# Kernel optimization log

Hardware: AMD Instinct MI355X
Metric: run time of the kernel (lower is better)

The kernel has to match this reference:

```python
import jax, jax.numpy as jnp
import numpy as np

N_LEVELS = 16
LOG2_T = 19
T = 1 << LOG2_T
BASE = 16
MAXRES = 4096
F = 2
MAXC = 16  # (max_SH_degree+1)^2
PER_LEVEL_SCALE = float(np.exp((np.log(MAXRES) - np.log(BASE)) / (N_LEVELS - 1)))
RES = jnp.asarray([BASE * PER_LEVEL_SCALE ** l for l in range(N_LEVELS)], dtype=jnp.float32)
PRIMES = jnp.array([1, 2654435761, 805459861], dtype=jnp.uint32)
OFFS = jnp.asarray([[(i >> 2) & 1, (i >> 1) & 1, i & 1] for i in range(8)], dtype=jnp.int32)  # (8,3)

C0 = 0.28209479177387814
C1 = 0.4886025119029199
C2 = (1.0925484305920792, -1.0925484305920792, 0.31539156525252005, -1.0925484305920792, 0.5462742152960396)
C3 = (-0.5900435899266435, 2.890611442640554, -0.4570457994644658, 0.3731763325901154, -0.4570457994644658, 1.445305721320277, -0.5900435899266435)


def hash_encode(x, table):
    # x: (N,3) in [0,1]; table: (L,T,F). Multiresolution hash grid (tcnn HashGrid).
    def level(tab, res):
        p = x * res
        p0 = jnp.floor(p)
        w = p - p0                                  # (N,3) trilerp weights
        c = p0.astype(jnp.uint32)[:, None, :] + OFFS[None].astype(jnp.uint32)  # (N,8,3)
        h = (c[..., 0] * PRIMES[0]) ^ (c[..., 1] * PRIMES[1]) ^ (c[..., 2] * PRIMES[2])
        idx = (h & jnp.uint32(T - 1)).astype(jnp.int32)
        f = tab[idx]                                # (N,8,F) irregular gather
        wc = jnp.where(OFFS[None].astype(bool), w[:, None, :], 1.0 - w[:, None, :]).prod(-1)
        return (f * wc[..., None]).sum(1)           # (N,F)
    feats = jax.vmap(level)(table, RES)             # (L,N,F)
    return feats.transpose(1, 0, 2).reshape(x.shape[0], N_LEVELS * F)


def sh_basis(d):
    # real SH basis up to degree 3; d: (N,3) unit vectors -> (N,16)
    x, y, z = d[..., 0], d[..., 1], d[..., 2]
    xx, yy, zz = x * x, y * y, z * z
    xy, yz, xz = x * y, y * z, x * z
    return jnp.stack([
        jnp.full_like(x, C0), -C1 * y, C1 * z, -C1 * x,
        C2[0] * xy, C2[1] * yz, C2[2] * (2 * zz - xx - yy), C2[3] * xz, C2[4] * (xx - yy),
        C3[0] * y * (3 * xx - yy), C3[1] * xy * z, C3[2] * y * (4 * zz - xx - yy),
        C3[3] * z * (2 * zz - 3 * xx - 3 * yy), C3[4] * x * (4 * zz - xx - yy),
        C3[5] * z * (xx - yy), C3[6] * x * (xx - 3 * yy)], axis=-1)


def network_forward(positions, rx_pos, table, W1, W2, aabb, active_deg):
    aabb_min, aabb_max = aabb[:3], aabb[3:]
    scale = jnp.maximum(aabb_max - aabb_min, 1e-6)
    norm_pos = (positions - aabb_min) / scale
    selector = jnp.all((norm_pos >= 0.0) & (norm_pos <= 1.0), axis=-1)  # (N,)
    pos_n = jnp.clip(norm_pos, 0.0, 1.0)  # safe values for masked-out points (zeroed below)

    def density_fn(pn):
        feats = hash_encode(pn, table)
        h = jax.nn.relu(feats @ W1)
        sh = (h @ W2).reshape(-1, MAXC, 2)
        dens = C0 * sh[:, 0, :]                     # (N,2) = (real, imag) of sigma
        return jnp.sqrt(dens[:, 0] ** 2 + dens[:, 1] ** 2).sum(), (dens, sh)

    # in-forward autograd: grad of sum |sigma| w.r.t. normalized positions
    (_, (dens, sh)), g = jax.value_and_grad(density_fn, has_aux=True)(pos_n)
    g_world = g / scale
    nrm = -g_world / jnp.maximum(jnp.linalg.norm(g_world, axis=-1, keepdims=True), 1e-20)
    nrm = jnp.where(jnp.isnan(nrm), 0.0, nrm)

    # EvalSH: view direction from sample point toward receiver, SH dot coefficients
    dirs = rx_pos - positions
    dirs = dirs / jnp.maximum(jnp.linalg.norm(dirs, axis=-1, keepdims=True), 1e-20)
    Y = sh_basis(dirs)                              # (N,16)
    mask = (jnp.arange(MAXC) < (active_deg + 1) ** 2).astype(Y.dtype)
    scat = jnp.einsum('nc,ncf->nf', Y * mask, sh)   # (N,2) complex as (re,im)

    sel = selector[:, None]
    dens = jnp.where(sel, dens, 0.0)
    scat = jnp.where(sel, scat, 0.0)
    nrm = jnp.where(sel, nrm, 0.0)
    shz = jnp.where(selector[:, None, None], sh, 0.0)
    # pack: sigma(re,im) | scatterers_to(re,im) | normals(3) | sh_coeffs(32) -> (N,39)
    return jnp.concatenate([dens, scat, nrm, shz.reshape(-1, MAXC * 2)], axis=-1)


def setup_inputs() -> dict:
    key = jax.random.key(0)
    ks = jax.random.split(key, 6)
    N = 262144
    positions = jax.random.uniform(ks[0], (N, 3), jnp.float32) * 2.2 - 1.1
    rx_pos = jax.random.normal(ks[1], (3,), jnp.float32) * 2.0
    table = (jax.random.uniform(ks[2], (N_LEVELS, T, F), jnp.float32) * 2.0 - 1.0) * 1e-4
    d_in, hid, d_out = N_LEVELS * F, 32, MAXC * 2
    W1 = jax.random.normal(ks[3], (d_in, hid), jnp.float32) / np.sqrt(d_in)
    W2 = jax.random.normal(ks[4], (hid, d_out), jnp.float32) / np.sqrt(hid)
    aabb = jnp.array([-1.0, -1.0, -1.0, 1.0, 1.0, 1.0], jnp.float32)
    return {"positions": positions, "rx_pos": rx_pos, "table": table, "W1": W1,
            "W2": W2, "aabb": aabb, "active_deg": 3}


def reference(positions, rx_pos, table, W1, W2, aabb, active_deg):
    return network_forward(positions, rx_pos, table, W1, W2, aabb, active_deg)
```

## Files before the change

kernel.cpp:

```cpp
#include <hip/hip_runtime.h>
#include <cmath>

#pragma clang fp contract(off)

#define NLV 16
#define TSZ (1u << 19)
#define TMASK (TSZ - 1u)
#define PR1 2654435761u
#define PR2 805459861u

typedef float v2f __attribute__((ext_vector_type(2)));
typedef float v4f __attribute__((ext_vector_type(4)));

struct ResT { float r[NLV]; };

__device__ __forceinline__ void aabb_norm(
    const float* __restrict__ g_aabb, float posx, float posy, float posz,
    float& s0, float& s1, float& s2,
    float& pnx, float& pny, float& pnz, bool& sel)
{
    float a0 = g_aabb[0], a1 = g_aabb[1], a2 = g_aabb[2];
    s0 = fmaxf(g_aabb[3] - a0, 1e-6f);
    s1 = fmaxf(g_aabb[4] - a1, 1e-6f);
    s2 = fmaxf(g_aabb[5] - a2, 1e-6f);
    float nx = (posx - a0) / s0;
    float ny = (posy - a1) / s1;
    float nz = (posz - a2) / s2;
    sel = (nx >= 0.f) && (nx <= 1.f) && (ny >= 0.f) && (ny <= 1.f)
       && (nz >= 0.f) && (nz <= 1.f);
    pnx = fminf(fmaxf(nx, 0.f), 1.f);
    pny = fminf(fmaxf(ny, 0.f), 1.f);
    pnz = fminf(fmaxf(nz, 0.f), 1.f);
}

__global__ __launch_bounds__(256) void level_gather(
    const float* __restrict__ g_pos,
    const float* __restrict__ g_tab,
    const float* __restrict__ g_aabb,
    float* __restrict__ ws,
    int N, int chunks, ResT rt)
{
    int b = blockIdx.x;
    int lvl = b / chunks;
    int n = (b - lvl * chunks) * 256 + threadIdx.x;
    if (n >= N) return;

    float posx = g_pos[3*n+0], posy = g_pos[3*n+1], posz = g_pos[3*n+2];
    float s0, s1, s2, pnx, pny, pnz; bool sel;
    aabb_norm(g_aabb, posx, posy, posz, s0, s1, s2, pnx, pny, pnz, sel);

    float res = rt.r[lvl];
    const float2* tl = (const float2*)g_tab + (size_t)lvl * TSZ;

    float fx = pnx * res, fy = pny * res, fz = pnz * res;
    float x0 = floorf(fx), y0 = floorf(fy), z0 = floorf(fz);
    float wx = fx - x0, wy = fy - y0, wz = fz - z0;
    float omx = 1.f - wx, omy = 1.f - wy, omz = 1.f - wz;
    unsigned ux = (unsigned)x0, uy = (unsigned)y0, uz = (unsigned)z0;
    unsigned hx0 = ux,        hx1 = ux + 1u;
    unsigned hy0 = uy * PR1,  hy1 = (uy + 1u) * PR1;
    unsigned hz0 = uz * PR2,  hz1 = (uz + 1u) * PR2;
    float f0 = 0.f, f1 = 0.f;
    float lxa = 0.f, lxb = 0.f, lya = 0.f, lyb = 0.f, lza = 0.f, lzb = 0.f;
#pragma unroll
    for (int c = 0; c < 8; ++c) {
        unsigned hh = ((c & 4) ? hx1 : hx0) ^ ((c & 2) ? hy1 : hy0) ^ ((c & 1) ? hz1 : hz0);
        float2 fv = tl[hh & TMASK];
        float wxv = (c & 4) ? wx : omx;
        float wyv = (c & 2) ? wy : omy;
        float wzv = (c & 1) ? wz : omz;
        float wgt = wxv * wyv;
        wgt = wgt * wzv;
        float t0 = fv.x * wgt;
        float t1 = fv.y * wgt;
        f0 = f0 + t0;
        f1 = f1 + t1;
        float pyz = wyv * wzv;
        float pxz = wxv * wzv;
        float pxy = wxv * wyv;
        float spx = (c & 4) ? pyz : -pyz;
        float spy = (c & 2) ? pxz : -pxz;
        float spz = (c & 1) ? pxy : -pxy;
        lxa = lxa + fv.x * spx;  lxb = lxb + fv.y * spx;
        lya = lya + fv.x * spy;  lyb = lyb + fv.y * spy;
        lza = lza + fv.x * spz;  lzb = lzb + fv.y * spz;
    }

    size_t LN = (size_t)NLV * N;
    size_t idx = (size_t)lvl * N + n;
    v2f* f2 = (v2f*)ws;
    v4f* p4 = (v4f*)(ws + 2*LN);
    v2f* p2 = (v2f*)(ws + 6*LN);
    v2f ff = {f0, f1};
    v4f pa = {lxa, lxb, lya, lyb};
    v2f pz = {lza, lzb};
    f2[idx] = ff;
    p4[idx] = pa;
    p2[idx] = pz;
}

__global__ __launch_bounds__(256) void mlp_bwd(
    const float* __restrict__ g_pos,
    const float* __restrict__ g_rx,
    const float* __restrict__ g_W1,
    const float* __restrict__ g_W2,
    const float* __restrict__ g_aabb,
    const int*   __restrict__ g_deg,
    const float* __restrict__ ws,
    float* __restrict__ g_out,
    int N, ResT rt)
{
    int n = blockIdx.x * 256 + threadIdx.x;
    if (n >= N) return;

    float posx = g_pos[3*n+0], posy = g_pos[3*n+1], posz = g_pos[3*n+2];
    float s0, s1, s2, pnx, pny, pnz; bool sel;
    aabb_norm(g_aabb, posx, posy, posz, s0, s1, s2, pnx, pny, pnz, sel);
    (void)pnx; (void)pny; (void)pnz;

    size_t LN = (size_t)NLV * N;
    const v2f* f2 = (const v2f*)ws;
    const v4f* p4 = (const v4f*)(ws + 2*LN);
    const v2f* p2 = (const v2f*)(ws + 6*LN);

    float z1[32];
#pragma unroll
    for (int i = 0; i < 32; ++i) z1[i] = 0.f;
    for (int l = 0; l < NLV; ++l) {
        v2f fv = f2[(size_t)l * N + n];
        float f0 = fv.x;
        float f1 = fv.y;
        const float* w1a = g_W1 + (2*l) * 32;
        const float* w1b = g_W1 + (2*l+1) * 32;
#pragma unroll
        for (int i = 0; i < 32; ++i) {
            float acc = fmaf(f0, w1a[i], z1[i]);
            z1[i] = fmaf(f1, w1b[i], acc);
        }
    }

    unsigned mask = 0u;
    float sh[32];
#pragma unroll
    for (int o = 0; o < 32; ++o) sh[o] = 0.f;
#pragma unroll
    for (int i = 0; i < 32; ++i) {
        bool on = (z1[i] > 0.f);
        if (on) mask |= (1u << i);
        float h = on ? z1[i] : 0.f;
        const float* w2r = g_W2 + i * 32;
#pragma unroll
        for (int o = 0; o < 32; ++o) sh[o] = fmaf(h, w2r[o], sh[o]);
    }

    const float C0c = 0.28209479177387814f;
    float d0 = C0c * sh[0], d1 = C0c * sh[1];

    float rx0 = g_rx[0], rx1 = g_rx[1], rx2 = g_rx[2];
    float dxw = rx0 - posx, dyw = rx1 - posy, dzw = rx2 - posz;
    float dnorm = sqrtf(dxw*dxw + dyw*dyw + dzw*dzw);
    float dinv = 1.f / fmaxf(dnorm, 1e-20f);
    float X = dxw * dinv, Yd = dyw * dinv, Z = dzw * dinv;
    float xx = X*X, yy = Yd*Yd, zz = Z*Z;
    float xy = X*Yd, yz = Yd*Z, xz = X*Z;
    float Yb[16];
    Yb[0]  = 0.28209479177387814f;
    Yb[1]  = -0.4886025119029199f * Yd;
    Yb[2]  =  0.4886025119029199f * Z;
    Yb[3]  = -0.4886025119029199f * X;
    Yb[4]  =  1.0925484305920792f * xy;
    Yb[5]  = -1.0925484305920792f * yz;
    Yb[6]  =  0.31539156525252005f * (2.f*zz - xx - yy);
    Yb[7]  = -1.0925484305920792f * xz;
    Yb[8]  =  0.5462742152960396f * (xx - yy);
    Yb[9]  = -0.5900435899266435f * Yd * (3.f*xx - yy);
    Yb[10] =  2.890611442640554f  * xy * Z;
    Yb[11] = -0.4570457994644658f * Yd * (4.f*zz - xx - yy);
    Yb[12] =  0.3731763325901154f * Z * (2.f*zz - 3.f*xx - 3.f*yy);
    Yb[13] = -0.4570457994644658f * X * (4.f*zz - xx - yy);
    Yb[14] =  1.445305721320277f  * Z * (xx - yy);
    Yb[15] = -0.5900435899266435f * X * (xx - 3.f*yy);

    int deg = g_deg[0];
    int nact = (deg + 1) * (deg + 1);
    float sc0 = 0.f, sc1 = 0.f;
#pragma unroll
    for (int c = 0; c < 16; ++c) {
        float yc = (c < nact) ? Yb[c] : 0.f;
        sc0 = fmaf(yc, sh[2*c+0], sc0);
        sc1 = fmaf(yc, sh[2*c+1], sc1);
    }

    float* op = g_out + (size_t)n * 39;
    op[0] = sel ? d0  : 0.f;
    op[1] = sel ? d1  : 0.f;
    op[2] = sel ? sc0 : 0.f;
    op[3] = sel ? sc1 : 0.f;
#pragma unroll
    for (int c = 0; c < 32; ++c) op[7 + c] = sel ? sh[c] : 0.f;

    float ss = d0*d0 + d1*d1;
    float q0 = 0.f, q1 = 0.f;
    if (ss > 0.f) {
        float sr = sqrtf(ss);
        q0 = C0c * d0 / sr;
        q1 = C0c * d1 / sr;
    }
    float dzv[32];
#pragma unroll
    for (int i = 0; i < 32; ++i) {
        float dh = fmaf(q0, g_W2[i*32+0], q1 * g_W2[i*32+1]);
        dzv[i] = ((mask >> i) & 1u) ? dh : 0.f;
    }

    float gx = 0.f, gy = 0.f, gz = 0.f;
    const float4* w1v = (const float4*)g_W1;
    for (int l = 0; l < NLV; ++l) {
        v4f c4 = p4[(size_t)l * N + n];
        v2f c2 = p2[(size_t)l * N + n];
        const float4* wa = w1v + (size_t)(2*l) * 8;
        const float4* wb = wa + 8;
        float da = 0.f, db = 0.f;
#pragma unroll
        for (int k = 0; k < 8; ++k) {
            float4 va = wa[k], vb = wb[k];
            da = fmaf(va.x, dzv[4*k+0], da);
            da = fmaf(va.y, dzv[4*k+1], da);
            da = fmaf(va.z, dzv[4*k+2], da);
            da = fmaf(va.w, dzv[4*k+3], da);
            db = fmaf(vb.x, dzv[4*k+0], db);
            db = fmaf(vb.y, dzv[4*k+1], db);
            db = fmaf(vb.z, dzv[4*k+2], db);
            db = fmaf(vb.w, dzv[4*k+3], db);
        }
        float res = rt.r[l];
        gx = fmaf(res, fmaf(da, c4.x, db * c4.y), gx);
        gy = fmaf(res, fmaf(da, c4.z, db * c4.w), gy);
        gz = fmaf(res, fmaf(da, c2.x, db * c2.y), gz);
    }

    float gwx = gx / s0, gwy = gy / s1, gwz = gz / s2;
    float gn = sqrtf(gwx*gwx + gwy*gwy + gwz*gwz);
    float ginv = -1.f / fmaxf(gn, 1e-20f);
    op[4] = sel ? gwx * ginv : 0.f;
    op[5] = sel ? gwy * ginv : 0.f;
    op[6] = sel ? gwz * ginv : 0.f;
}

__global__ __launch_bounds__(256, 2) void ngp_fused(
    const float* __restrict__ g_pos,
    const float* __restrict__ g_rx,
    const float* __restrict__ g_tab,
    const float* __restrict__ g_W1,
    const float* __restrict__ g_W2,
    const float* __restrict__ g_aabb,
    const int*   __restrict__ g_deg,
    float* __restrict__ g_out,
    int N, ResT rt)
{
    __shared__ float sm[48][256];

    int tid = blockIdx.x * 256 + threadIdx.x;
    int lt  = threadIdx.x;
    int n = tid >> 1;
    int p = tid & 1;
    if (n >= N) return;

    float posx = g_pos[3*n+0], posy = g_pos[3*n+1], posz = g_pos[3*n+2];
    float s0, s1, s2, pnx, pny, pnz; bool sel;
    aabb_norm(g_aabb, posx, posy, posz, s0, s1, s2, pnx, pny, pnz, sel);

    const float2* tab = (const float2*)g_tab;
    float f0o[8], f1o[8];
#pragma unroll
    for (int j = 0; j < 8; ++j) {
        float res = p ? rt.r[8+j] : rt.r[j];
        const float2* tl = tab + (size_t)(p * 8 + j) * TSZ;
        float fx = pnx * res, fy = pny * res, fz = pnz * res;
        float x0 = floorf(fx), y0 = floorf(fy), z0 = floorf(fz);
        float wx = fx - x0, wy = fy - y0, wz = fz - z0;
        float omx = 1.f - wx, omy = 1.f - wy, omz = 1.f - wz;
        unsigned ux = (unsigned)x0, uy = (unsigned)y0, uz = (unsigned)z0;
        unsigned hx0 = ux,        hx1 = ux + 1u;
        unsigned hy0 = uy * PR1,  hy1 = (uy + 1u) * PR1;
        unsigned hz0 = uz * PR2,  hz1 = (uz + 1u) * PR2;
        float f0 = 0.f, f1 = 0.f;
        float lxa = 0.f, lxb = 0.f, lya = 0.f, lyb = 0.f, lza = 0.f, lzb = 0.f;
#pragma unroll
        for (int c = 0; c < 8; ++c) {
            unsigned hh = ((c & 4) ? hx1 : hx0) ^ ((c & 2) ? hy1 : hy0) ^ ((c & 1) ? hz1 : hz0);
            float2 fv = tl[hh & TMASK];
            float wxv = (c & 4) ? wx : omx;
            float wyv = (c & 2) ? wy : omy;
            float wzv = (c & 1) ? wz : omz;
            float wgt = wxv * wyv;
            wgt = wgt * wzv;
            float t0 = fv.x * wgt;
            float t1 = fv.y * wgt;
            f0 = f0 + t0;
            f1 = f1 + t1;
            float pyz = wyv * wzv;
            float pxz = wxv * wzv;
            float pxy = wxv * wyv;
            float spx = (c & 4) ? pyz : -pyz;
            float spy = (c & 2) ? pxz : -pxz;
            float spz = (c & 1) ? pxy : -pxy;
            lxa = lxa + fv.x * spx;  lxb = lxb + fv.y * spx;
            lya = lya + fv.x * spy;  lyb = lyb + fv.y * spy;
            lza = lza + fv.x * spz;  lzb = lzb + fv.y * spz;
        }
        f0o[j] = f0; f1o[j] = f1;
        sm[j*6+0][lt] = lxa;  sm[j*6+1][lt] = lxb;
        sm[j*6+2][lt] = lya;  sm[j*6+3][lt] = lyb;
        sm[j*6+4][lt] = lza;  sm[j*6+5][lt] = lzb;
    }

    float z1[32];
#pragma unroll
    for (int i = 0; i < 32; ++i) z1[i] = 0.f;
    float hi0[8], hi1[8];
#pragma unroll
    for (int j = 0; j < 8; ++j) {
        float t0 = __shfl_xor(f0o[j], 1, 64);
        float t1 = __shfl_xor(f1o[j], 1, 64);
        float lo0 = p ? t0 : f0o[j];
        float lo1 = p ? t1 : f1o[j];
        hi0[j] = p ? f0o[j] : t0;
        hi1[j] = p ? f1o[j] : t1;
        const float* w1a = g_W1 + (2*j) * 32;
        const float* w1b = g_W1 + (2*j+1) * 32;
#pragma unroll
        for (int i = 0; i < 32; ++i) {
            float acc = fmaf(lo0, w1a[i], z1[i]);
            z1[i] = fmaf(lo1, w1b[i], acc);
        }
    }
#pragma unroll
    for (int j = 0; j < 8; ++j) {
        const float* w1a = g_W1 + (2*(8+j)) * 32;
        const float* w1b = g_W1 + (2*(8+j)+1) * 32;
#pragma unroll
        for (int i = 0; i < 32; ++i) {
            float acc = fmaf(hi0[j], w1a[i], z1[i]);
            z1[i] = fmaf(hi1[j], w1b[i], acc);
        }
    }

    unsigned mask = 0u;
    float sh[32];
#pragma unroll
    for (int o = 0; o < 32; ++o) sh[o] = 0.f;
#pragma unroll
    for (int i = 0; i < 32; ++i) {
        bool on = (z1[i] > 0.f);
        if (on) mask |= (1u << i);
        float h = on ? z1[i] : 0.f;
        const float* w2r = g_W2 + i * 32;
#pragma unroll
        for (int o = 0; o < 32; ++o) sh[o] = fmaf(h, w2r[o], sh[o]);
    }

    const float C0c = 0.28209479177387814f;
    float d0 = C0c * sh[0], d1 = C0c * sh[1];

    float rx0 = g_rx[0], rx1 = g_rx[1], rx2 = g_rx[2];
    float dxw = rx0 - posx, dyw = rx1 - posy, dzw = rx2 - posz;
    float dnorm = sqrtf(dxw*dxw + dyw*dyw + dzw*dzw);
    float dinv = 1.f / fmaxf(dnorm, 1e-20f);
    float X = dxw * dinv, Yd = dyw * dinv, Z = dzw * dinv;
    float xx = X*X, yy = Yd*Yd, zz = Z*Z;
    float xy = X*Yd, yz = Yd*Z, xz = X*Z;
    float Yb[16];
    Yb[0]  = 0.28209479177387814f;
    Yb[1]  = -0.4886025119029199f * Yd;
    Yb[2]  =  0.4886025119029199f * Z;
    Yb[3]  = -0.4886025119029199f * X;
    Yb[4]  =  1.0925484305920792f * xy;
    Yb[5]  = -1.0925484305920792f * yz;
    Yb[6]  =  0.31539156525252005f * (2.f*zz - xx - yy);
    Yb[7]  = -1.0925484305920792f * xz;
    Yb[8]  =  0.5462742152960396f * (xx - yy);
    Yb[9]  = -0.5900435899266435f * Yd * (3.f*xx - yy);
    Yb[10] =  2.890611442640554f  * xy * Z;
    Yb[11] = -0.4570457994644658f * Yd * (4.f*zz - xx - yy);
    Yb[12] =  0.3731763325901154f * Z * (2.f*zz - 3.f*xx - 3.f*yy);
    Yb[13] = -0.4570457994644658f * X * (4.f*zz - xx - yy);
    Yb[14] =  1.445305721320277f  * Z * (xx - yy);
    Yb[15] = -0.5900435899266435f * X * (xx - 3.f*yy);

    int deg = g_deg[0];
    int nact = (deg + 1) * (deg + 1);
    float sc0 = 0.f, sc1 = 0.f;
#pragma unroll
    for (int c = 0; c < 16; ++c) {
        float yc = (c < nact) ? Yb[c] : 0.f;
        sc0 = fmaf(yc, sh[2*c+0], sc0);
        sc1 = fmaf(yc, sh[2*c+1], sc1);
    }

    float* op = g_out + (size_t)n * 39;
    if (p == 0) {
        op[0] = sel ? d0  : 0.f;
        op[1] = sel ? d1  : 0.f;
        op[2] = sel ? sc0 : 0.f;
        op[3] = sel ? sc1 : 0.f;
#pragma unroll
        for (int c = 0; c < 13; ++c) op[7 + c] = sel ? sh[c] : 0.f;
    } else {
#pragma unroll
        for (int c = 13; c < 32; ++c) op[7 + c] = sel ? sh[c] : 0.f;
    }

    float ss = d0*d0 + d1*d1;
    float q0 = 0.f, q1 = 0.f;
    if (ss > 0.f) {
        float sr = sqrtf(ss);
        q0 = C0c * d0 / sr;
        q1 = C0c * d1 / sr;
    }
    float dzv[32];
#pragma unroll
    for (int i = 0; i < 32; ++i) {
        float dh = fmaf(q0, g_W2[i*32+0], q1 * g_W2[i*32+1]);
        dzv[i] = ((mask >> i) & 1u) ? dh : 0.f;
    }

    float gx = 0.f, gy = 0.f, gz = 0.f;
    const float4* w1v = (const float4*)g_W1;
    int rbase = p * 16;
#pragma unroll
    for (int j = 0; j < 8; ++j) {
        const float4* wa = w1v + (size_t)(rbase + 2*j) * 8;
        const float4* wb = wa + 8;
        float da = 0.f, db = 0.f;
#pragma unroll
        for (int k = 0; k < 8; ++k) {
            float4 va = wa[k], vb = wb[k];
            da = fmaf(va.x, dzv[4*k+0], da);
            da = fmaf(va.y, dzv[4*k+1], da);
            da = fmaf(va.z, dzv[4*k+2], da);
            da = fmaf(va.w, dzv[4*k+3], da);
            db = fmaf(vb.x, dzv[4*k+0], db);
            db = fmaf(vb.y, dzv[4*k+1], db);
            db = fmaf(vb.z, dzv[4*k+2], db);
            db = fmaf(vb.w, dzv[4*k+3], db);
        }
        float xa = sm[j*6+0][lt], xb = sm[j*6+1][lt];
        float ya = sm[j*6+2][lt], yb = sm[j*6+3][lt];
        float za = sm[j*6+4][lt], zb = sm[j*6+5][lt];
        float res = p ? rt.r[8+j] : rt.r[j];
        gx = fmaf(res, fmaf(da, xa, db * xb), gx);
        gy = fmaf(res, fmaf(da, ya, db * yb), gy);
        gz = fmaf(res, fmaf(da, za, db * zb), gz);
    }
    float tx = __shfl_xor(gx, 1, 64);
    float ty = __shfl_xor(gy, 1, 64);
    float tz = __shfl_xor(gz, 1, 64);
    gx = gx + tx; gy = gy + ty; gz = gz + tz;

    float gwx = gx / s0, gwy = gy / s1, gwz = gz / s2;
    float gn = sqrtf(gwx*gwx + gwy*gwy + gwz*gwz);
    float ginv = -1.f / fmaxf(gn, 1e-20f);
    if (p == 0) {
        op[4] = sel ? gwx * ginv : 0.f;
        op[5] = sel ? gwy * ginv : 0.f;
        op[6] = sel ? gwz * ginv : 0.f;
    }
}

extern "C" void kernel_launch(void* const* d_in, const int* in_sizes, int n_in,
                              void* d_out, int out_size, void* d_ws, size_t ws_size,
                              hipStream_t stream)
{
    const float* g_pos  = (const float*)d_in[0];
    const float* g_rx   = (const float*)d_in[1];
    const float* g_tab  = (const float*)d_in[2];
    const float* g_W1   = (const float*)d_in[3];
    const float* g_W2   = (const float*)d_in[4];
    const float* g_aabb = (const float*)d_in[5];
    const int*   g_deg  = (const int*)d_in[6];
    float* g_out = (float*)d_out;

    int N = in_sizes[0] / 3;

    ResT rt;
    double scale = exp((log(4096.0) - log(16.0)) / 15.0);
    for (int l = 0; l < NLV; ++l) rt.r[l] = (float)(16.0 * pow(scale, (double)l));

    size_t need = (size_t)NLV * N * 8 * sizeof(float);
    if (ws_size >= need) {
        float* ws = (float*)d_ws;
        int chunks = (N + 255) / 256;
        level_gather<<<NLV * chunks, 256, 0, stream>>>(g_pos, g_tab, g_aabb,
                                                       ws, N, chunks, rt);
        mlp_bwd<<<chunks, 256, 0, stream>>>(g_pos, g_rx, g_W1, g_W2, g_aabb,
                                            g_deg, ws, g_out, N, rt);
    } else {
        long long threads = 2LL * N;
        int blocks = (int)((threads + 255) / 256);
        ngp_fused<<<blocks, 256, 0, stream>>>(g_pos, g_rx, g_tab, g_W1, g_W2,
                                              g_aabb, g_deg, g_out, N, rt);
    }
}
```

Measured before the change: 381.8 us.

## Interleave level blocks, stream workspace stores, and prefetch workspace loads in MLP

The gather kernel now maps consecutive blocks to 8 different levels over the same point chunk, so position loads are shared in cache and eight table slices are gathered concurrently. Workspace writes use nontemporal stores to avoid polluting cache. The MLP/backward kernel issues workspace loads for the first four levels up front and keeps a four-deep rolling prefetch while fully unrolling the level loops, to hide global load latency. The added prefetch registers raise register pressure and may cut occupancy.

```diff
diff --git a/kernel.cpp b/kernel.cpp
--- a/kernel.cpp
+++ b/kernel.cpp
@@ -41,8 +41,10 @@
     int N, int chunks, ResT rt)
 {
     int b = blockIdx.x;
-    int lvl = b / chunks;
-    int n = (b - lvl * chunks) * 256 + threadIdx.x;
+    int half = (b >= 8 * chunks) ? 1 : 0;
+    int bb = b - half * (8 * chunks);
+    int lvl = (bb & 7) + (half << 3);
+    int n = (bb >> 3) * 256 + threadIdx.x;
     if (n >= N) return;
 
     float posx = g_pos[3*n+0], posy = g_pos[3*n+1], posz = g_pos[3*n+2];
@@ -94,9 +96,9 @@
     v2f ff = {f0, f1};
     v4f pa = {lxa, lxb, lya, lyb};
     v2f pz = {lza, lzb};
-    f2[idx] = ff;
-    p4[idx] = pa;
-    p2[idx] = pz;
+    __builtin_nontemporal_store(ff, f2 + idx);
+    __builtin_nontemporal_store(pa, p4 + idx);
+    __builtin_nontemporal_store(pz, p2 + idx);
 }
 
 __global__ __launch_bounds__(256) void mlp_bwd(
@@ -113,23 +115,36 @@
     int n = blockIdx.x * 256 + threadIdx.x;
     if (n >= N) return;
 
+    size_t LN = (size_t)NLV * N;
+    const v2f* f2 = (const v2f*)ws;
+    const v4f* p4 = (const v4f*)(ws + 2*LN);
+    const v2f* p2 = (const v2f*)(ws + 6*LN);
+
+    v2f fv[4];
+#pragma unroll
+    for (int j = 0; j < 4; ++j) fv[j] = f2[(size_t)j * N + n];
+    v4f pc4[4];
+    v2f pc2[4];
+#pragma unroll
+    for (int j = 0; j < 4; ++j) {
+        pc4[j] = p4[(size_t)j * N + n];
+        pc2[j] = p2[(size_t)j * N + n];
+    }
+
     float posx = g_pos[3*n+0], posy = g_pos[3*n+1], posz = g_pos[3*n+2];
     float s0, s1, s2, pnx, pny, pnz; bool sel;
     aabb_norm(g_aabb, posx, posy, posz, s0, s1, s2, pnx, pny, pnz, sel);
     (void)pnx; (void)pny; (void)pnz;
 
-    size_t LN = (size_t)NLV * N;
-    const v2f* f2 = (const v2f*)ws;
-    const v4f* p4 = (const v4f*)(ws + 2*LN);
-    const v2f* p2 = (const v2f*)(ws + 6*LN);
-
     float z1[32];
 #pragma unroll
     for (int i = 0; i < 32; ++i) z1[i] = 0.f;
+#pragma unroll
     for (int l = 0; l < NLV; ++l) {
-        v2f fv = f2[(size_t)l * N + n];
-        float f0 = fv.x;
-        float f1 = fv.y;
+        v2f fvl = fv[l & 3];
+        if (l + 4 < NLV) fv[l & 3] = f2[(size_t)(l + 4) * N + n];
+        float f0 = fvl.x;
+        float f1 = fvl.y;
         const float* w1a = g_W1 + (2*l) * 32;
         const float* w1b = g_W1 + (2*l+1) * 32;
 #pragma unroll
@@ -215,9 +230,14 @@
 
     float gx = 0.f, gy = 0.f, gz = 0.f;
     const float4* w1v = (const float4*)g_W1;
+#pragma unroll
     for (int l = 0; l < NLV; ++l) {
-        v4f c4 = p4[(size_t)l * N + n];
-        v2f c2 = p2[(size_t)l * N + n];
+        v4f c4 = pc4[l & 3];
+        v2f c2 = pc2[l & 3];
+        if (l + 4 < NLV) {
+            pc4[l & 3] = p4[(size_t)(l + 4) * N + n];
+            pc2[l & 3] = p2[(size_t)(l + 4) * N + n];
+        }
         const float4* wa = w1v + (size_t)(2*l) * 8;
         const float4* wb = wa + 8;
         float da = 0.f, db = 0.f;
```

Result: faster. 334.6 us (-12.4%).
